# Kernel optimization log

Measured on AMD Instinct MI355X. Metric: run time of the kernel, lower is better.

Reference implementation:

```python
import jax, jax.numpy as jnp
import numpy as np

B, T, C, U, W = 8, 2048, 512, 512, 2


def setup_inputs() -> dict:
    key = jax.random.key(0)
    k1, k2 = jax.random.split(key)
    x = jax.random.normal(k1, (B, T, C), dtype=jnp.float32)
    # Conv1D kernel: [window, in_channels, 3*units] (z, f, o gates), glorot-ish scale
    kernel = jax.random.normal(k2, (W, C, 3 * U), dtype=jnp.float32) * (1.0 / np.sqrt(W * C))
    bias = jnp.zeros((3 * U,), dtype=jnp.float32)
    initial_state = jnp.zeros((1, U), dtype=jnp.float32)
    return {"x": x, "kernel": kernel, "bias": bias, "initial_state": initial_state}


def reference(x, kernel, bias, initial_state):
    # Causal Conv1D: pad (window-1) on the left of the time axis.
    window = kernel.shape[0]
    gates = jax.lax.conv_general_dilated(
        x, kernel,
        window_strides=(1,),
        padding=[(window - 1, 0)],
        dimension_numbers=("NWC", "WIO", "NWC"),
    ) + bias  # [B, T, 3U]
    z, f, o = jnp.split(gates, 3, axis=-1)
    z = jnp.tanh(z)
    f = jax.nn.sigmoid(f)
    o = jax.nn.sigmoid(o)

    # fo-pool recurrence: h_t = f_t * h_{t-1} + (1 - f_t) * z_t
    h0 = jnp.repeat(initial_state, x.shape[0], axis=0)  # [B, U]
    fs = jnp.moveaxis(f, 1, 0)  # [T, B, U]
    zs = jnp.moveaxis(z, 1, 0)  # [T, B, U]

    def step(h, fz):
        f_t, z_t = fz
        h = f_t * h + (1.0 - f_t) * z_t
        return h, h

    _, hs = jax.lax.scan(step, h0, (fs, zs))  # hs: [T, B, U]
    recurrent = jnp.moveaxis(hs, 0, 1)  # [B, T, U]

    # output gate, return_sequences=True
    return recurrent * o
```

## Files before the change

### kernel.cpp

```cpp
#include <hip/hip_runtime.h>


#define Bn 8
#define Tn 2048
#define Cn 512
#define Un 512
#define Nn 1536
#define Kn 1024
#define Mn (Bn * Tn)
#define NC 32
#define CL 64

using bf16x8 = __attribute__((ext_vector_type(8))) __bf16;
using f32x4  = __attribute__((ext_vector_type(4))) float;
using us8    = __attribute__((ext_vector_type(8))) unsigned short;

__device__ __forceinline__ void async16(const void* g, void* l) {
  __builtin_amdgcn_global_load_lds((const __attribute__((address_space(1))) void*)g,
                                   (__attribute__((address_space(3))) void*)l, 16, 0, 0);
}

__device__ __forceinline__ unsigned short f2bf(float v) {
  union { float f; unsigned u; } c; c.f = v;
  unsigned u = c.u;
  return (unsigned short)((u + 0x7fffu + ((u >> 16) & 1u)) >> 16);
}
__device__ __forceinline__ float asf(unsigned u) {
  union { unsigned u; float f; } c; c.u = u; return c.f;
}
__device__ __forceinline__ float bf_lo(unsigned w) { return asf(w << 16); }
__device__ __forceinline__ float bf_hi(unsigned w) { return asf(w & 0xffff0000u); }

__device__ __forceinline__ float fast_sigmoid(float x) {
  float e = __builtin_amdgcn_exp2f(-1.4426950408889634f * x);
  return __builtin_amdgcn_rcpf(1.0f + e);
}
__device__ __forceinline__ float fast_tanh(float x) {
  float e = __builtin_amdgcn_exp2f(-2.8853900817779268f * x);
  return 2.0f * __builtin_amdgcn_rcpf(1.0f + e) - 1.0f;
}

__global__ __launch_bounds__(256) void conv_x(const float* __restrict__ x,
                                              unsigned short* __restrict__ xb) {
  int idx = blockIdx.x * 256 + threadIdx.x;
  int c8  = idx & 63;
  int row = idx >> 6;
  int b   = row / (Tn + 1);
  int t   = row - b * (Tn + 1);
  us8 ov;
  if (t == 0) {
    ov = (us8)0;
  } else {
    const float* src = x + (size_t)(b * Tn + t - 1) * Cn + c8 * 8;
    float4 v0 = *(const float4*)src;
    float4 v1 = *(const float4*)(src + 4);
    ov[0] = f2bf(v0.x); ov[1] = f2bf(v0.y); ov[2] = f2bf(v0.z); ov[3] = f2bf(v0.w);
    ov[4] = f2bf(v1.x); ov[5] = f2bf(v1.y); ov[6] = f2bf(v1.z); ov[7] = f2bf(v1.w);
  }
  *(us8*)(xb + (size_t)row * Cn + c8 * 8) = ov;
}

__global__ __launch_bounds__(256) void conv_k(const float* __restrict__ kern,
                                              unsigned short* __restrict__ kT) {
  __shared__ float tile[32][33];
  int kb = blockIdx.x, nb = blockIdx.y;
  int tx = threadIdx.x & 31, ty = threadIdx.x >> 5;
#pragma unroll
  for (int i = 0; i < 4; i++)
    tile[ty + i * 8][tx] = kern[(size_t)(kb * 32 + ty + i * 8) * Nn + nb * 32 + tx];
  __syncthreads();
#pragma unroll
  for (int i = 0; i < 4; i++) {
    int n = nb * 32 + ty + i * 8;
    int k = kb * 32 + tx;
    kT[(size_t)n * Kn + k] = f2bf(tile[tx][ty + i * 8]);
  }
}

__global__ __launch_bounds__(256) void gemm_gates(const unsigned short* __restrict__ xb,
                                                  const unsigned short* __restrict__ kT,
                                                  const float* __restrict__ bias,
                                                  unsigned short* __restrict__ gates) {
  __shared__ unsigned short As[128 * 64];
  __shared__ unsigned short Bs[128 * 64];
  const int tid = threadIdx.x;
  const int m0 = blockIdx.x * 128;
  const int n0 = blockIdx.y * 128;
  const int batch = m0 / Tn;
  const int lane = tid & 63;
  const int w = tid >> 6, wr = w >> 1, wc = w & 1;

  const int srow = (w << 3) + (lane >> 3);
  const int skq  = (lane & 7) ^ (lane >> 3);
  const unsigned short* aStage = xb + (size_t)(m0 + batch + srow) * Cn + (skq << 3);
  const unsigned short* bStage = kT + (size_t)(n0 + srow) * Kn + (skq << 3);

  f32x4 zero = {0.f, 0.f, 0.f, 0.f};
  f32x4 acc[4][4];
#pragma unroll
  for (int i = 0; i < 4; i++)
#pragma unroll
    for (int j = 0; j < 4; j++) acc[i][j] = zero;

  const int rA0 = wr * 64 + (lane & 15);
  const int rB0 = wc * 64 + (lane & 15);
  const int swz = lane & 7;

  for (int k0 = 0; k0 < Kn; k0 += 64) {
#pragma unroll
    for (int j = 0; j < 4; j++) {
      async16(aStage + (size_t)(j << 5) * Cn + k0, &As[(j * 256 + tid) * 8]);
      async16(bStage + (size_t)(j << 5) * Kn + k0, &Bs[(j * 256 + tid) * 8]);
    }
    __builtin_amdgcn_s_waitcnt(0);
    __syncthreads();

#pragma unroll
    for (int ks = 0; ks < 2; ks++) {
      const int col = (((ks << 2) + (lane >> 4)) ^ swz) << 3;
      bf16x8 af[4], bf[4];
#pragma unroll
      for (int i = 0; i < 4; i++) {
        af[i] = *(const bf16x8*)&As[(rA0 + i * 16) * 64 + col];
        bf[i] = *(const bf16x8*)&Bs[(rB0 + i * 16) * 64 + col];
      }
#pragma unroll
      for (int i = 0; i < 4; i++)
#pragma unroll
        for (int j = 0; j < 4; j++)
          acc[i][j] = __builtin_amdgcn_mfma_f32_16x16x32_bf16(af[i], bf[j], acc[i][j], 0, 0, 0);
    }
    __syncthreads();
  }

  const int region = blockIdx.y >> 2;
  const int rowB = wr * 64 + (lane >> 4) * 4;
  const int colB = wc * 64 + (lane & 15);
#pragma unroll
  for (int i = 0; i < 4; i++)
#pragma unroll
    for (int j = 0; j < 4; j++)
#pragma unroll
      for (int r = 0; r < 4; r++) {
        int mm = m0 + rowB + i * 16 + r;
        int nn = n0 + colB + j * 16;
        float g = acc[i][j][r] + bias[nn];
        float a = (region == 0) ? fast_tanh(g) : fast_sigmoid(g);
        gates[(size_t)mm * Nn + nn] = f2bf(a);
      }
}

__global__ __launch_bounds__(256) void scan_phaseA(const unsigned short* __restrict__ gates,
                                                   unsigned int* __restrict__ ab) {
  int chunk = blockIdx.x;
  int b = chunk >> 5, c = chunk & (NC - 1);
  int u2 = threadIdx.x * 2;
  const unsigned short* gp = gates + (size_t)(b * Tn + c * CL) * Nn;
  float a0 = 1.f, a1 = 1.f, bv0 = 0.f, bv1 = 0.f;
#pragma unroll 8
  for (int t = 0; t < CL; t++) {
    unsigned zz = *(const unsigned*)(gp + u2);
    unsigned ff = *(const unsigned*)(gp + Un + u2);
    float z0 = bf_lo(zz), z1 = bf_hi(zz);
    float f0 = bf_lo(ff), f1 = bf_hi(ff);
    a0 *= f0; a1 *= f1;
    bv0 = f0 * bv0 + (1.0f - f0) * z0;
    bv1 = f1 * bv1 + (1.0f - f1) * z1;
    gp += Nn;
  }
  uint2 w;
  w.x = ((unsigned)f2bf(a0) << 16) | f2bf(bv0);
  w.y = ((unsigned)f2bf(a1) << 16) | f2bf(bv1);
  *(uint2*)(ab + (size_t)chunk * Un + u2) = w;
}

__global__ __launch_bounds__(256) void scan_phaseC(const unsigned short* __restrict__ gates,
                                                   const unsigned int* __restrict__ ab,
                                                   const float* __restrict__ init,
                                                   float* __restrict__ out) {
  int chunk = blockIdx.x;
  int b = chunk >> 5, c = chunk & (NC - 1);
  int u2 = threadIdx.x * 2;
  float h0 = init[u2], h1 = init[u2 + 1];
  for (int cp = 0; cp < c; cp++) {
    uint2 w = *(const uint2*)(ab + (size_t)(b * NC + cp) * Un + u2);
    h0 = asf(w.x & 0xffff0000u) * h0 + bf_lo(w.x);
    h1 = asf(w.y & 0xffff0000u) * h1 + bf_lo(w.y);
  }
  const unsigned short* gp = gates + (size_t)(b * Tn + c * CL) * Nn;
  float* op = out + (size_t)(b * Tn + c * CL) * Un;
#pragma unroll 8
  for (int t = 0; t < CL; t++) {
    unsigned zz = *(const unsigned*)(gp + u2);
    unsigned ff = *(const unsigned*)(gp + Un + u2);
    unsigned oo = *(const unsigned*)(gp + 2 * Un + u2);
    float z0 = bf_lo(zz), z1 = bf_hi(zz);
    float f0 = bf_lo(ff), f1 = bf_hi(ff);
    float o0 = bf_lo(oo), o1 = bf_hi(oo);
    h0 = f0 * h0 + (1.0f - f0) * z0;
    h1 = f1 * h1 + (1.0f - f1) * z1;
    float2 ov; ov.x = h0 * o0; ov.y = h1 * o1;
    *(float2*)(op + u2) = ov;
    gp += Nn;
    op += Un;
  }
}

extern "C" void kernel_launch(void* const* d_in, const int* in_sizes, int n_in,
                              void* d_out, int out_size, void* d_ws, size_t ws_size,
                              hipStream_t stream) {
  const float* x    = (const float*)d_in[0];
  const float* kern = (const float*)d_in[1];
  const float* bias = (const float*)d_in[2];
  const float* init = (const float*)d_in[3];
  float* out = (float*)d_out;

  char* ws = (char*)d_ws;
  unsigned short* xb = (unsigned short*)ws;
  size_t off = (size_t)Bn * (Tn + 1) * Cn * 2;
  unsigned short* kT = (unsigned short*)(ws + off);
  off += (size_t)Nn * Kn * 2;
  unsigned short* gates = (unsigned short*)(ws + off);
  off += (size_t)Mn * Nn * 2;
  unsigned int* ab = (unsigned int*)(ws + off);

  conv_x<<<(Bn * (Tn + 1) * Cn / 8) / 256, 256, 0, stream>>>(x, xb);
  conv_k<<<dim3(32, 48), 256, 0, stream>>>(kern, kT);
  gemm_gates<<<dim3(Mn / 128, Nn / 128), 256, 0, stream>>>(xb, kT, bias, gates);
  scan_phaseA<<<Bn * NC, 256, 0, stream>>>(gates, ab);
  scan_phaseC<<<Bn * NC, 256, 0, stream>>>(gates, ab, init, out);
}
```

Before: 178.1 us.

## Fuse all stages into one cooperative persistent kernel with grid syncs

Replaces the five kernel launches with a single cooperative kernel of 512 blocks. It runs the weight transpose and input conversion, then the gates GEMM (three N-tiles per block), then the two scan phases, separated by grid-wide syncs. The goal is to remove launch gaps and per-kernel tail effects. The scans now use one unit per thread over twice as many blocks, which means narrower 2-byte loads. The GEMM grid is also serialised to 3 tiles per block, and grid.sync adds its own overhead.

```diff
diff --git a/kernel.cpp b/kernel.cpp
--- a/kernel.cpp
+++ b/kernel.cpp
@@ -1,5 +1,8 @@
 #include <hip/hip_runtime.h>
-
+#include <hip/hip_cooperative_groups.h>
+
+
+namespace cg = cooperative_groups;
 
 #define Bn 8
 #define Tn 2048
@@ -28,8 +31,8 @@
 __device__ __forceinline__ float asf(unsigned u) {
   union { unsigned u; float f; } c; c.u = u; return c.f;
 }
+__device__ __forceinline__ float bf2f(unsigned short h) { return asf(((unsigned)h) << 16); }
 __device__ __forceinline__ float bf_lo(unsigned w) { return asf(w << 16); }
-__device__ __forceinline__ float bf_hi(unsigned w) { return asf(w & 0xffff0000u); }
 
 __device__ __forceinline__ float fast_sigmoid(float x) {
   float e = __builtin_amdgcn_exp2f(-1.4426950408889634f * x);
@@ -38,6 +41,175 @@
 __device__ __forceinline__ float fast_tanh(float x) {
   float e = __builtin_amdgcn_exp2f(-2.8853900817779268f * x);
   return 2.0f * __builtin_amdgcn_rcpf(1.0f + e) - 1.0f;
+}
+
+__global__ __launch_bounds__(256, 2) void qrnn_fused(const float* __restrict__ x,
+                                                     const float* __restrict__ kern,
+                                                     const float* __restrict__ bias,
+                                                     const float* __restrict__ init,
+                                                     unsigned short* __restrict__ xb,
+                                                     unsigned short* __restrict__ kT,
+                                                     unsigned short* __restrict__ gates,
+                                                     unsigned int* __restrict__ ab,
+                                                     float* __restrict__ out) {
+  cg::grid_group grid = cg::this_grid();
+  __shared__ unsigned short As[128 * 64];
+  __shared__ unsigned short Bs[128 * 64];
+  const int tid = threadIdx.x;
+  const int blk = blockIdx.x;
+
+  {
+    float (*tileF)[33] = (float(*)[33])As;
+    int tx = tid & 31, ty = tid >> 5;
+    for (int tile = blk; tile < 1536; tile += 512) {
+      int kb = tile & 31, nb = tile >> 5;
+#pragma unroll
+      for (int i = 0; i < 4; i++)
+        tileF[ty + i * 8][tx] = kern[(size_t)(kb * 32 + ty + i * 8) * Nn + nb * 32 + tx];
+      __syncthreads();
+#pragma unroll
+      for (int i = 0; i < 4; i++)
+        kT[(size_t)(nb * 32 + ty + i * 8) * Kn + kb * 32 + tx] = f2bf(tileF[tx][ty + i * 8]);
+      __syncthreads();
+    }
+  }
+
+  {
+    const int total = Bn * (Tn + 1) * Cn / 8;
+    for (int idx = blk * 256 + tid; idx < total; idx += 512 * 256) {
+      int c8  = idx & 63;
+      int row = idx >> 6;
+      int b   = row / (Tn + 1);
+      int t   = row - b * (Tn + 1);
+      us8 ov;
+      if (t == 0) {
+        ov = (us8)0;
+      } else {
+        const float* src = x + (size_t)(b * Tn + t - 1) * Cn + c8 * 8;
+        float4 v0 = *(const float4*)src;
+        float4 v1 = *(const float4*)(src + 4);
+        ov[0] = f2bf(v0.x); ov[1] = f2bf(v0.y); ov[2] = f2bf(v0.z); ov[3] = f2bf(v0.w);
+        ov[4] = f2bf(v1.x); ov[5] = f2bf(v1.y); ov[6] = f2bf(v1.z); ov[7] = f2bf(v1.w);
+      }
+      *(us8*)(xb + (size_t)row * Cn + c8 * 8) = ov;
+    }
+  }
+
+  grid.sync();
+
+  {
+    const int lane = tid & 63;
+    const int w = tid >> 6, wr = w >> 1, wc = w & 1;
+    const int my = blk & 127;
+    const int m0 = my * 128;
+    const int batch = my >> 4;
+    const int srow = (w << 3) + (lane >> 3);
+    const int skq  = (lane & 7) ^ (lane >> 3);
+    const unsigned short* aStage = xb + (size_t)(m0 + batch + srow) * Cn + (skq << 3);
+    const int rA0 = wr * 64 + (lane & 15);
+    const int rB0 = wc * 64 + (lane & 15);
+    const int swz = lane & 7;
+
+#pragma unroll 1
+    for (int i = 0; i < 3; i++) {
+      const int id = blk + 512 * i;
+      const int ny = id >> 7;
+      const int n0 = ny * 128;
+      const unsigned short* bStage = kT + (size_t)(n0 + srow) * Kn + (skq << 3);
+
+      f32x4 zero = {0.f, 0.f, 0.f, 0.f};
+      f32x4 acc[4][4];
+#pragma unroll
+      for (int a = 0; a < 4; a++)
+#pragma unroll
+        for (int b2 = 0; b2 < 4; b2++) acc[a][b2] = zero;
+
+      for (int k0 = 0; k0 < Kn; k0 += 64) {
+#pragma unroll
+        for (int j = 0; j < 4; j++) {
+          async16(aStage + (size_t)(j << 5) * Cn + k0, &As[(j * 256 + tid) * 8]);
+          async16(bStage + (size_t)(j << 5) * Kn + k0, &Bs[(j * 256 + tid) * 8]);
+        }
+        __builtin_amdgcn_s_waitcnt(0);
+        __syncthreads();
+#pragma unroll
+        for (int ks = 0; ks < 2; ks++) {
+          const int col = (((ks << 2) + (lane >> 4)) ^ swz) << 3;
+          bf16x8 af[4], bf[4];
+#pragma unroll
+          for (int a = 0; a < 4; a++) {
+            af[a] = *(const bf16x8*)&As[(rA0 + a * 16) * 64 + col];
+            bf[a] = *(const bf16x8*)&Bs[(rB0 + a * 16) * 64 + col];
+          }
+#pragma unroll
+          for (int a = 0; a < 4; a++)
+#pragma unroll
+            for (int b2 = 0; b2 < 4; b2++)
+              acc[a][b2] = __builtin_amdgcn_mfma_f32_16x16x32_bf16(af[a], bf[b2], acc[a][b2], 0, 0, 0);
+        }
+        __syncthreads();
+      }
+
+      const int rowB = wr * 64 + (lane >> 4) * 4;
+      const int colB = wc * 64 + (lane & 15);
+#pragma unroll
+      for (int a = 0; a < 4; a++)
+#pragma unroll
+        for (int b2 = 0; b2 < 4; b2++)
+#pragma unroll
+          for (int r = 0; r < 4; r++) {
+            int mm = m0 + rowB + a * 16 + r;
+            int nn = n0 + colB + b2 * 16;
+            float g = acc[a][b2][r] + bias[nn];
+            float v = (i == 0) ? fast_tanh(g) : fast_sigmoid(g);
+            gates[(size_t)mm * Nn + nn] = f2bf(v);
+          }
+    }
+  }
+
+  grid.sync();
+
+  {
+    int chunk = blk >> 1;
+    int u = (blk & 1) * 256 + tid;
+    int b = chunk >> 5, c = chunk & (NC - 1);
+    const unsigned short* gp = gates + (size_t)(b * Tn + c * CL) * Nn;
+    float a = 1.0f, bv = 0.0f;
+#pragma unroll 8
+    for (int t = 0; t < CL; t++) {
+      float z = bf2f(gp[u]);
+      float f = bf2f(gp[Un + u]);
+      a *= f;
+      bv = f * bv + (1.0f - f) * z;
+      gp += Nn;
+    }
+    ab[(size_t)chunk * Un + u] = ((unsigned)f2bf(a) << 16) | f2bf(bv);
+  }
+
+  grid.sync();
+
+  {
+    int chunk = blk >> 1;
+    int u = (blk & 1) * 256 + tid;
+    int b = chunk >> 5, c = chunk & (NC - 1);
+    float h = init[u];
+    for (int cp = 0; cp < c; cp++) {
+      unsigned wv = ab[(size_t)(b * NC + cp) * Un + u];
+      h = asf(wv & 0xffff0000u) * h + bf_lo(wv);
+    }
+    const unsigned short* gp = gates + (size_t)(b * Tn + c * CL) * Nn;
+    float* op = out + (size_t)(b * Tn + c * CL) * Un;
+#pragma unroll 8
+    for (int t = 0; t < CL; t++) {
+      float z = bf2f(gp[u]);
+      float f = bf2f(gp[Un + u]);
+      float o = bf2f(gp[2 * Un + u]);
+      h = f * h + (1.0f - f) * z;
+      op[u] = h * o;
+      gp += Nn;
+      op += Un;
+    }
+  }
 }
 
 __global__ __launch_bounds__(256) void conv_x(const float* __restrict__ x,
@@ -152,55 +324,43 @@
 
 __global__ __launch_bounds__(256) void scan_phaseA(const unsigned short* __restrict__ gates,
                                                    unsigned int* __restrict__ ab) {
-  int chunk = blockIdx.x;
+  int chunk = blockIdx.x >> 1;
+  int u = (blockIdx.x & 1) * 256 + threadIdx.x;
   int b = chunk >> 5, c = chunk & (NC - 1);
-  int u2 = threadIdx.x * 2;
   const unsigned short* gp = gates + (size_t)(b * Tn + c * CL) * Nn;
-  float a0 = 1.f, a1 = 1.f, bv0 = 0.f, bv1 = 0.f;
+  float a = 1.0f, bv = 0.0f;
 #pragma unroll 8
   for (int t = 0; t < CL; t++) {
-    unsigned zz = *(const unsigned*)(gp + u2);
-    unsigned ff = *(const unsigned*)(gp + Un + u2);
-    float z0 = bf_lo(zz), z1 = bf_hi(zz);
-    float f0 = bf_lo(ff), f1 = bf_hi(ff);
-    a0 *= f0; a1 *= f1;
-    bv0 = f0 * bv0 + (1.0f - f0) * z0;
-    bv1 = f1 * bv1 + (1.0f - f1) * z1;
+    float z = bf2f(gp[u]);
+    float f = bf2f(gp[Un + u]);
+    a *= f;
+    bv = f * bv + (1.0f - f) * z;
     gp += Nn;
   }
-  uint2 w;
-  w.x = ((unsigned)f2bf(a0) << 16) | f2bf(bv0);
-  w.y = ((unsigned)f2bf(a1) << 16) | f2bf(bv1);
-  *(uint2*)(ab + (size_t)chunk * Un + u2) = w;
+  ab[(size_t)chunk * Un + u] = ((unsigned)f2bf(a) << 16) | f2bf(bv);
 }
 
 __global__ __launch_bounds__(256) void scan_phaseC(const unsigned short* __restrict__ gates,
                                                    const unsigned int* __restrict__ ab,
                                                    const float* __restrict__ init,
                                                    float* __restrict__ out) {
-  int chunk = blockIdx.x;
+  int chunk = blockIdx.x >> 1;
+  int u = (blockIdx.x & 1) * 256 + threadIdx.x;
   int b = chunk >> 5, c = chunk & (NC - 1);
-  int u2 = threadIdx.x * 2;
-  float h0 = init[u2], h1 = init[u2 + 1];
+  float h = init[u];
   for (int cp = 0; cp < c; cp++) {
-    uint2 w = *(const uint2*)(ab + (size_t)(b * NC + cp) * Un + u2);
-    h0 = asf(w.x & 0xffff0000u) * h0 + bf_lo(w.x);
-    h1 = asf(w.y & 0xffff0000u) * h1 + bf_lo(w.y);
+    unsigned wv = ab[(size_t)(b * NC + cp) * Un + u];
+    h = asf(wv & 0xffff0000u) * h + bf_lo(wv);
   }
   const unsigned short* gp = gates + (size_t)(b * Tn + c * CL) * Nn;
   float* op = out + (size_t)(b * Tn + c * CL) * Un;
 #pragma unroll 8
   for (int t = 0; t < CL; t++) {
-    unsigned zz = *(const unsigned*)(gp + u2);
-    unsigned ff = *(const unsigned*)(gp + Un + u2);
-    unsigned oo = *(const unsigned*)(gp + 2 * Un + u2);
-    float z0 = bf_lo(zz), z1 = bf_hi(zz);
-    float f0 = bf_lo(ff), f1 = bf_hi(ff);
-    float o0 = bf_lo(oo), o1 = bf_hi(oo);
-    h0 = f0 * h0 + (1.0f - f0) * z0;
-    h1 = f1 * h1 + (1.0f - f1) * z1;
-    float2 ov; ov.x = h0 * o0; ov.y = h1 * o1;
-    *(float2*)(op + u2) = ov;
+    float z = bf2f(gp[u]);
+    float f = bf2f(gp[Un + u]);
+    float o = bf2f(gp[2 * Un + u]);
+    h = f * h + (1.0f - f) * z;
+    op[u] = h * o;
     gp += Nn;
     op += Un;
   }
@@ -224,9 +384,15 @@
   off += (size_t)Mn * Nn * 2;
   unsigned int* ab = (unsigned int*)(ws + off);
 
-  conv_x<<<(Bn * (Tn + 1) * Cn / 8) / 256, 256, 0, stream>>>(x, xb);
-  conv_k<<<dim3(32, 48), 256, 0, stream>>>(kern, kT);
-  gemm_gates<<<dim3(Mn / 128, Nn / 128), 256, 0, stream>>>(xb, kT, bias, gates);
-  scan_phaseA<<<Bn * NC, 256, 0, stream>>>(gates, ab);
-  scan_phaseC<<<Bn * NC, 256, 0, stream>>>(gates, ab, init, out);
-}
+  void* args[] = {(void*)&x, (void*)&kern, (void*)&bias, (void*)&init,
+                  (void*)&xb, (void*)&kT, (void*)&gates, (void*)&ab, (void*)&out};
+  hipError_t e = hipLaunchCooperativeKernel(qrnn_fused, dim3(512), dim3(256),
+                                            args, 0, stream);
+  if (e != hipSuccess) {
+    conv_x<<<(Bn * (Tn + 1) * Cn / 8) / 256, 256, 0, stream>>>(x, xb);
+    conv_k<<<dim3(32, 48), 256, 0, stream>>>(kern, kT);
+    gemm_gates<<<dim3(Mn / 128, Nn / 128), 256, 0, stream>>>(xb, kT, bias, gates);
+    scan_phaseA<<<Bn * NC * 2, 256, 0, stream>>>(gates, ab);
+    scan_phaseC<<<Bn * NC * 2, 256, 0, stream>>>(gates, ab, init, out);
+  }
+}
```

After: 354.3 us. 1.99x slower.

## Fuse chunk-local scan into gate GEMM and merge prep kernels

Applied to the files above, without the earlier changes.

Merges the x and kernel conversion kernels into one launch, and restructures the GEMM so each block computes z, f and o tiles for the same rows sequentially, keeping z and f in LDS to run the chunk-local scan (phase A) in-kernel. This removes the separate phase A pass over gates and a couple of launches. Phase C is rewritten to process one unit per thread over twice as many blocks. The trade-off is a GEMM grid one third as large with more LDS per block, reducing parallelism and occupancy.

```diff
diff --git a/kernel.cpp b/kernel.cpp
--- a/kernel.cpp
+++ b/kernel.cpp
@@ -28,8 +28,8 @@
 __device__ __forceinline__ float asf(unsigned u) {
   union { unsigned u; float f; } c; c.u = u; return c.f;
 }
+__device__ __forceinline__ float bf2f(unsigned short h) { return asf(((unsigned)h) << 16); }
 __device__ __forceinline__ float bf_lo(unsigned w) { return asf(w << 16); }
-__device__ __forceinline__ float bf_hi(unsigned w) { return asf(w & 0xffff0000u); }
 
 __device__ __forceinline__ float fast_sigmoid(float x) {
   float e = __builtin_amdgcn_exp2f(-1.4426950408889634f * x);
@@ -40,167 +40,170 @@
   return 2.0f * __builtin_amdgcn_rcpf(1.0f + e) - 1.0f;
 }
 
-__global__ __launch_bounds__(256) void conv_x(const float* __restrict__ x,
-                                              unsigned short* __restrict__ xb) {
-  int idx = blockIdx.x * 256 + threadIdx.x;
-  int c8  = idx & 63;
-  int row = idx >> 6;
-  int b   = row / (Tn + 1);
-  int t   = row - b * (Tn + 1);
-  us8 ov;
-  if (t == 0) {
-    ov = (us8)0;
+__global__ __launch_bounds__(256) void prep(const float* __restrict__ x,
+                                            const float* __restrict__ kern,
+                                            unsigned short* __restrict__ xb,
+                                            unsigned short* __restrict__ kT) {
+  __shared__ float tile[32][33];
+  const int tid = threadIdx.x;
+  if (blockIdx.x < 1536) {
+    int kb = blockIdx.x & 31, nb = blockIdx.x >> 5;
+    int tx = tid & 31, ty = tid >> 5;
+#pragma unroll
+    for (int i = 0; i < 4; i++)
+      tile[ty + i * 8][tx] = kern[(size_t)(kb * 32 + ty + i * 8) * Nn + nb * 32 + tx];
+    __syncthreads();
+#pragma unroll
+    for (int i = 0; i < 4; i++) {
+      int n = nb * 32 + ty + i * 8;
+      int k = kb * 32 + tx;
+      kT[(size_t)n * Kn + k] = f2bf(tile[tx][ty + i * 8]);
+    }
   } else {
-    const float* src = x + (size_t)(b * Tn + t - 1) * Cn + c8 * 8;
-    float4 v0 = *(const float4*)src;
-    float4 v1 = *(const float4*)(src + 4);
-    ov[0] = f2bf(v0.x); ov[1] = f2bf(v0.y); ov[2] = f2bf(v0.z); ov[3] = f2bf(v0.w);
-    ov[4] = f2bf(v1.x); ov[5] = f2bf(v1.y); ov[6] = f2bf(v1.z); ov[7] = f2bf(v1.w);
-  }
-  *(us8*)(xb + (size_t)row * Cn + c8 * 8) = ov;
-}
-
-__global__ __launch_bounds__(256) void conv_k(const float* __restrict__ kern,
-                                              unsigned short* __restrict__ kT) {
-  __shared__ float tile[32][33];
-  int kb = blockIdx.x, nb = blockIdx.y;
-  int tx = threadIdx.x & 31, ty = threadIdx.x >> 5;
-#pragma unroll
-  for (int i = 0; i < 4; i++)
-    tile[ty + i * 8][tx] = kern[(size_t)(kb * 32 + ty + i * 8) * Nn + nb * 32 + tx];
-  __syncthreads();
-#pragma unroll
-  for (int i = 0; i < 4; i++) {
-    int n = nb * 32 + ty + i * 8;
-    int k = kb * 32 + tx;
-    kT[(size_t)n * Kn + k] = f2bf(tile[tx][ty + i * 8]);
-  }
-}
-
-__global__ __launch_bounds__(256) void gemm_gates(const unsigned short* __restrict__ xb,
+    int idx = (blockIdx.x - 1536) * 256 + tid;
+    int c8  = idx & 63;
+    int row = idx >> 6;
+    int b   = row / (Tn + 1);
+    int t   = row - b * (Tn + 1);
+    us8 ov;
+    if (t == 0) {
+      ov = (us8)0;
+    } else {
+      const float* src = x + (size_t)(b * Tn + t - 1) * Cn + c8 * 8;
+      float4 v0 = *(const float4*)src;
+      float4 v1 = *(const float4*)(src + 4);
+      ov[0] = f2bf(v0.x); ov[1] = f2bf(v0.y); ov[2] = f2bf(v0.z); ov[3] = f2bf(v0.w);
+      ov[4] = f2bf(v1.x); ov[5] = f2bf(v1.y); ov[6] = f2bf(v1.z); ov[7] = f2bf(v1.w);
+    }
+    *(us8*)(xb + (size_t)row * Cn + c8 * 8) = ov;
+  }
+}
+
+__global__ __launch_bounds__(256) void gemm3_scan(const unsigned short* __restrict__ xb,
                                                   const unsigned short* __restrict__ kT,
                                                   const float* __restrict__ bias,
-                                                  unsigned short* __restrict__ gates) {
+                                                  unsigned short* __restrict__ gates,
+                                                  unsigned int* __restrict__ ab) {
   __shared__ unsigned short As[128 * 64];
   __shared__ unsigned short Bs[128 * 64];
+  __shared__ unsigned short Zs[128 * 128];
+  unsigned short* Fs = As;
+
   const int tid = threadIdx.x;
-  const int m0 = blockIdx.x * 128;
-  const int n0 = blockIdx.y * 128;
-  const int batch = m0 / Tn;
+  const int my = blockIdx.x;
+  const int nsub = blockIdx.y;
+  const int m0 = my * 128;
+  const int batch = my >> 4;
   const int lane = tid & 63;
   const int w = tid >> 6, wr = w >> 1, wc = w & 1;
 
   const int srow = (w << 3) + (lane >> 3);
   const int skq  = (lane & 7) ^ (lane >> 3);
   const unsigned short* aStage = xb + (size_t)(m0 + batch + srow) * Cn + (skq << 3);
-  const unsigned short* bStage = kT + (size_t)(n0 + srow) * Kn + (skq << 3);
-
-  f32x4 zero = {0.f, 0.f, 0.f, 0.f};
-  f32x4 acc[4][4];
-#pragma unroll
-  for (int i = 0; i < 4; i++)
-#pragma unroll
-    for (int j = 0; j < 4; j++) acc[i][j] = zero;
-
   const int rA0 = wr * 64 + (lane & 15);
   const int rB0 = wc * 64 + (lane & 15);
   const int swz = lane & 7;
-
-  for (int k0 = 0; k0 < Kn; k0 += 64) {
-#pragma unroll
-    for (int j = 0; j < 4; j++) {
-      async16(aStage + (size_t)(j << 5) * Cn + k0, &As[(j * 256 + tid) * 8]);
-      async16(bStage + (size_t)(j << 5) * Kn + k0, &Bs[(j * 256 + tid) * 8]);
-    }
-    __builtin_amdgcn_s_waitcnt(0);
-    __syncthreads();
-
-#pragma unroll
-    for (int ks = 0; ks < 2; ks++) {
-      const int col = (((ks << 2) + (lane >> 4)) ^ swz) << 3;
-      bf16x8 af[4], bf[4];
-#pragma unroll
-      for (int i = 0; i < 4; i++) {
-        af[i] = *(const bf16x8*)&As[(rA0 + i * 16) * 64 + col];
-        bf[i] = *(const bf16x8*)&Bs[(rB0 + i * 16) * 64 + col];
-      }
-#pragma unroll
-      for (int i = 0; i < 4; i++)
-#pragma unroll
-        for (int j = 0; j < 4; j++)
-          acc[i][j] = __builtin_amdgcn_mfma_f32_16x16x32_bf16(af[i], bf[j], acc[i][j], 0, 0, 0);
-    }
-    __syncthreads();
-  }
-
-  const int region = blockIdx.y >> 2;
   const int rowB = wr * 64 + (lane >> 4) * 4;
   const int colB = wc * 64 + (lane & 15);
-#pragma unroll
-  for (int i = 0; i < 4; i++)
-#pragma unroll
-    for (int j = 0; j < 4; j++)
-#pragma unroll
-      for (int r = 0; r < 4; r++) {
-        int mm = m0 + rowB + i * 16 + r;
-        int nn = n0 + colB + j * 16;
-        float g = acc[i][j][r] + bias[nn];
-        float a = (region == 0) ? fast_tanh(g) : fast_sigmoid(g);
-        gates[(size_t)mm * Nn + nn] = f2bf(a);
+
+#pragma unroll 1
+  for (int reg = 0; reg < 3; reg++) {
+    const int n0 = reg * 512 + nsub * 128;
+    const unsigned short* bStage = kT + (size_t)(n0 + srow) * Kn + (skq << 3);
+
+    f32x4 zero = {0.f, 0.f, 0.f, 0.f};
+    f32x4 acc[4][4];
+#pragma unroll
+    for (int i = 0; i < 4; i++)
+#pragma unroll
+      for (int j = 0; j < 4; j++) acc[i][j] = zero;
+
+    for (int k0 = 0; k0 < Kn; k0 += 64) {
+#pragma unroll
+      for (int j = 0; j < 4; j++) {
+        async16(aStage + (size_t)(j << 5) * Cn + k0, &As[(j * 256 + tid) * 8]);
+        async16(bStage + (size_t)(j << 5) * Kn + k0, &Bs[(j * 256 + tid) * 8]);
       }
-}
-
-__global__ __launch_bounds__(256) void scan_phaseA(const unsigned short* __restrict__ gates,
-                                                   unsigned int* __restrict__ ab) {
-  int chunk = blockIdx.x;
-  int b = chunk >> 5, c = chunk & (NC - 1);
-  int u2 = threadIdx.x * 2;
-  const unsigned short* gp = gates + (size_t)(b * Tn + c * CL) * Nn;
-  float a0 = 1.f, a1 = 1.f, bv0 = 0.f, bv1 = 0.f;
+      __builtin_amdgcn_s_waitcnt(0);
+      __syncthreads();
+
+#pragma unroll
+      for (int ks = 0; ks < 2; ks++) {
+        const int col = (((ks << 2) + (lane >> 4)) ^ swz) << 3;
+        bf16x8 af[4], bf[4];
+#pragma unroll
+        for (int i = 0; i < 4; i++) {
+          af[i] = *(const bf16x8*)&As[(rA0 + i * 16) * 64 + col];
+          bf[i] = *(const bf16x8*)&Bs[(rB0 + i * 16) * 64 + col];
+        }
+#pragma unroll
+        for (int i = 0; i < 4; i++)
+#pragma unroll
+          for (int j = 0; j < 4; j++)
+            acc[i][j] = __builtin_amdgcn_mfma_f32_16x16x32_bf16(af[i], bf[j], acc[i][j], 0, 0, 0);
+      }
+      __syncthreads();
+    }
+
+#pragma unroll
+    for (int i = 0; i < 4; i++)
+#pragma unroll
+      for (int j = 0; j < 4; j++)
+#pragma unroll
+        for (int r = 0; r < 4; r++) {
+          int rl = rowB + i * 16 + r;
+          int ul = colB + j * 16;
+          int mm = m0 + rl;
+          int nn = n0 + ul;
+          float g = acc[i][j][r] + bias[nn];
+          float a = (reg == 0) ? fast_tanh(g) : fast_sigmoid(g);
+          unsigned short hb = f2bf(a);
+          gates[(size_t)mm * Nn + nn] = hb;
+          if (reg == 0) Zs[rl * 128 + ul] = hb;
+          else if (reg == 1) Fs[rl * 128 + ul] = hb;
+        }
+
+    if (reg == 1) {
+      __syncthreads();
+      int u  = tid & 127;
+      int ch = tid >> 7;
+      float a = 1.0f, bv = 0.0f;
 #pragma unroll 8
-  for (int t = 0; t < CL; t++) {
-    unsigned zz = *(const unsigned*)(gp + u2);
-    unsigned ff = *(const unsigned*)(gp + Un + u2);
-    float z0 = bf_lo(zz), z1 = bf_hi(zz);
-    float f0 = bf_lo(ff), f1 = bf_hi(ff);
-    a0 *= f0; a1 *= f1;
-    bv0 = f0 * bv0 + (1.0f - f0) * z0;
-    bv1 = f1 * bv1 + (1.0f - f1) * z1;
-    gp += Nn;
-  }
-  uint2 w;
-  w.x = ((unsigned)f2bf(a0) << 16) | f2bf(bv0);
-  w.y = ((unsigned)f2bf(a1) << 16) | f2bf(bv1);
-  *(uint2*)(ab + (size_t)chunk * Un + u2) = w;
+      for (int t = 0; t < CL; t++) {
+        float z = bf2f(Zs[(ch * 64 + t) * 128 + u]);
+        float f = bf2f(Fs[(ch * 64 + t) * 128 + u]);
+        a *= f;
+        bv = f * bv + (1.0f - f) * z;
+      }
+      int cglob = (my & 15) * 2 + ch;
+      ab[(size_t)(batch * NC + cglob) * Un + nsub * 128 + u] =
+          ((unsigned)f2bf(a) << 16) | f2bf(bv);
+      __syncthreads();
+    }
+  }
 }
 
 __global__ __launch_bounds__(256) void scan_phaseC(const unsigned short* __restrict__ gates,
                                                    const unsigned int* __restrict__ ab,
                                                    const float* __restrict__ init,
                                                    float* __restrict__ out) {
-  int chunk = blockIdx.x;
+  int chunk = blockIdx.x >> 1;
+  int u = (blockIdx.x & 1) * 256 + threadIdx.x;
   int b = chunk >> 5, c = chunk & (NC - 1);
-  int u2 = threadIdx.x * 2;
-  float h0 = init[u2], h1 = init[u2 + 1];
+  float h = init[u];
   for (int cp = 0; cp < c; cp++) {
-    uint2 w = *(const uint2*)(ab + (size_t)(b * NC + cp) * Un + u2);
-    h0 = asf(w.x & 0xffff0000u) * h0 + bf_lo(w.x);
-    h1 = asf(w.y & 0xffff0000u) * h1 + bf_lo(w.y);
+    unsigned wv = ab[(size_t)(b * NC + cp) * Un + u];
+    h = asf(wv & 0xffff0000u) * h + bf_lo(wv);
   }
   const unsigned short* gp = gates + (size_t)(b * Tn + c * CL) * Nn;
   float* op = out + (size_t)(b * Tn + c * CL) * Un;
 #pragma unroll 8
   for (int t = 0; t < CL; t++) {
-    unsigned zz = *(const unsigned*)(gp + u2);
-    unsigned ff = *(const unsigned*)(gp + Un + u2);
-    unsigned oo = *(const unsigned*)(gp + 2 * Un + u2);
-    float z0 = bf_lo(zz), z1 = bf_hi(zz);
-    float f0 = bf_lo(ff), f1 = bf_hi(ff);
-    float o0 = bf_lo(oo), o1 = bf_hi(oo);
-    h0 = f0 * h0 + (1.0f - f0) * z0;
-    h1 = f1 * h1 + (1.0f - f1) * z1;
-    float2 ov; ov.x = h0 * o0; ov.y = h1 * o1;
-    *(float2*)(op + u2) = ov;
+    float z = bf2f(gp[u]);
+    float f = bf2f(gp[Un + u]);
+    float o = bf2f(gp[2 * Un + u]);
+    h = f * h + (1.0f - f) * z;
+    op[u] = h * o;
     gp += Nn;
     op += Un;
   }
@@ -224,9 +227,7 @@
   off += (size_t)Mn * Nn * 2;
   unsigned int* ab = (unsigned int*)(ws + off);
 
-  conv_x<<<(Bn * (Tn + 1) * Cn / 8) / 256, 256, 0, stream>>>(x, xb);
-  conv_k<<<dim3(32, 48), 256, 0, stream>>>(kern, kT);
-  gemm_gates<<<dim3(Mn / 128, Nn / 128), 256, 0, stream>>>(xb, kT, bias, gates);
-  scan_phaseA<<<Bn * NC, 256, 0, stream>>>(gates, ab);
-  scan_phaseC<<<Bn * NC, 256, 0, stream>>>(gates, ab, init, out);
-}
+  prep<<<1536 + (Bn * (Tn + 1) * Cn / 8) / 256, 256, 0, stream>>>(x, kern, xb, kT);
+  gemm3_scan<<<dim3(128, 4), 256, 0, stream>>>(xb, kT, bias, gates, ab);
+  scan_phaseC<<<Bn * NC * 2, 256, 0, stream>>>(gates, ab, init, out);
+}
```

New measurement: 254.3 us. 1.43x slower.
